# Kernel optimization log

Measured on AMD Instinct MI355X. Metric: run time of the kernel, lower is better.

## Reference

```python
import jax, jax.numpy as jnp
import numpy as np

A_DIM = 6
VBR = jnp.array([300.0, 750.0, 1200.0, 1850.0, 2850.0, 4300.0])
MAX_BR = 4300.0
BUF = 30000.0  # buffer_size fixed to 30000 each forward
N_STEPS = 6    # unrolled iterations in the source (cooked_bw[0]..cooked_bw[5])


def _conv_feat(x, w, b):
    # 1-channel valid Conv1d(kernel=4) + ReLU, flattened channel-major like torch .view
    L = x.shape[0]
    idx = jnp.arange(L - 3)[:, None] + jnp.arange(4)[None, :]
    win = x[idx]                                   # (L-3, 4)
    out = jax.nn.relu(win @ w[:, 0, :].T + b)      # (L-3, 128)
    return out.T.reshape(-1)                       # (128*(L-3),)


def setup_inputs() -> dict:
    key = jax.random.key(0)
    ks = jax.random.split(key, 12)
    s = 0.1
    return {
        "inp": jax.random.uniform(ks[0], (8, 8), jnp.float32) + 0.1,
        "conv_w": jax.random.normal(ks[1], (128, 1, 4), jnp.float32) * s,
        "conv_b": jax.random.normal(ks[2], (128,), jnp.float32) * s,
        "w0": jax.random.normal(ks[3], (128, 1), jnp.float32) * s,
        "b0": jax.random.normal(ks[4], (128,), jnp.float32) * s,
        "w1": jax.random.normal(ks[5], (128, 1), jnp.float32) * s,
        "b1": jax.random.normal(ks[6], (128,), jnp.float32) * s,
        "w2": jax.random.normal(ks[7], (128, 1), jnp.float32) * s,
        "b2": jax.random.normal(ks[8], (128,), jnp.float32) * s,
        "w3": jax.random.normal(ks[9], (128, 2048), jnp.float32) * 0.02,
        "b3": jax.random.normal(ks[10], (128,), jnp.float32) * s,
        "w4": jax.random.normal(ks[11], (6, 128), jnp.float32) * s,
        "b4": jnp.zeros((6,), jnp.float32),
    }


def reference(inp, conv_w, conv_b, w0, b0, w1, b1, w2, b2, w3, b3, w4, b4):
    state = inp[:6, :]          # (6, 8)
    bw = inp[6, :]              # cooked bandwidth trace
    vs = inp[7, 0]              # base video chunk size
    vcs = vs * jnp.array([1.0, 2.0, 4.0, 8.0, 16.0, 32.0])  # video_chunk_sizes

    def net(st):
        s0 = jax.nn.relu(st[0, -1] * w0[:, 0] + b0)
        s1 = jax.nn.relu(st[1, -1] * w1[:, 0] + b1)
        s2 = _conv_feat(st[2, :], conv_w, conv_b)          # 640
        s3 = _conv_feat(st[3, :], conv_w, conv_b)          # 640
        s4 = _conv_feat(st[4, :A_DIM], conv_w, conv_b)     # 384
        s5 = st[4, -1] * w2[:, 0] + b2                     # no relu (matches source)
        feat = jnp.concatenate([s0, s1, s2, s3, s4, s5])   # (2048,)
        h = jax.nn.relu(w3 @ feat + b3)
        return w4 @ h + b4                                 # (6,)

    for i in range(N_STEPS):
        logits = net(state)
        a = jnp.argmax(logits)
        state = jnp.roll(state, -1, axis=1)
        delay = vcs[a] / bw[i] - BUF
        state = state.at[0, -1].set(VBR[a] / MAX_BR)
        state = state.at[1, -1].set(BUF / 1000.0 / 10.0)
        state = state.at[2, -1].set(vcs[a] / delay / 1000.0)
        state = state.at[3, -1].set(delay / 1000.0 / 10.0)
        state = state.at[4, :A_DIM].set(vcs / 1e6)
        state = state.at[5, -1].set((7.0 - i) / 8.0)

    return net(state)
```

## Files before the change

kernel.cpp:

```cpp
#include <hip/hip_runtime.h>

#define NBLK 32
#define TPB  256
#define FSTRIDE 32
#define PSTRIDE 64

__device__ __forceinline__ float relu_(float x) { return fmaxf(x, 0.f); }


__launch_bounds__(TPB, 1)
__global__ void actor_kernel(
    const float* __restrict__ inp,
    const float* __restrict__ conv_w, const float* __restrict__ conv_b,
    const float* __restrict__ w0, const float* __restrict__ b0,
    const float* __restrict__ w1, const float* __restrict__ b1,
    const float* __restrict__ w2, const float* __restrict__ b2,
    const float* __restrict__ w3, const float* __restrict__ b3,
    const float* __restrict__ w4, const float* __restrict__ b4,
    float* __restrict__ out, int* __restrict__ flags,
    float* __restrict__ partials)
{
    const int tid = threadIdx.x;
    const int b   = blockIdx.x;

    __shared__ __align__(16) float lw3[4 * 2048];
    __shared__ __align__(16) float lfeat[2048];
    __shared__ __align__(16) float lc2[512], lc3[512];
    __shared__ float lbase2[128], lbase3[128], ls5[128];
    __shared__ float ls0[6 * 128];
    __shared__ float ltmp[512];
    __shared__ __align__(16) float lcw[512];
    __shared__ float lcb[128];
    __shared__ float lw0v[128], lb0v[128], lw1v[128], lb1v[128];
    __shared__ float lw2v[128], lb2v[128], lb3v[128];
    __shared__ float lw4[768], lb4v[8];
    __shared__ float st2[8], st3[8], st4[8];
    __shared__ float sx[8];
    __shared__ float lbw[8];
    __shared__ float h_lds[4], hv_lds[4 * 8];
    __shared__ float red[48];
    __shared__ float sval[32 * 48];
    __shared__ float s_red[192];
    __shared__ int   sact[2];

    {
        const float4* g4 = (const float4*)(w3 + b * 4 * 2048);
        float4* l4 = (float4*)lw3;
        for (int idx = tid; idx < 2048; idx += TPB) l4[idx] = g4[idx];
    }
    for (int idx = tid; idx < 512; idx += TPB) lcw[idx] = conv_w[idx];
    if (tid < 128) {
        lcb[tid]  = conv_b[tid];
        lw0v[tid] = w0[tid]; lb0v[tid] = b0[tid];
        lw1v[tid] = w1[tid]; lb1v[tid] = b1[tid];
        lw2v[tid] = w2[tid]; lb2v[tid] = b2[tid];
        lb3v[tid] = b3[tid];
    }
    for (int idx = tid; idx < 768; idx += TPB) lw4[idx] = w4[idx];
    if (tid < 6) lb4v[tid] = b4[tid];
    if (tid < 8) {
        st2[tid] = inp[16 + tid];
        st3[tid] = inp[24 + tid];
        st4[tid] = inp[32 + tid];
        lbw[tid] = inp[48 + tid];
    }
    if (tid == 0) {
        sx[0] = inp[7];   sx[1] = inp[15];
        sx[2] = inp[39];  sx[3] = inp[32];
        sx[4] = inp[56];
    }
    __syncthreads();

    if (tid < 128) {
        const float vb[6] = {300.f, 750.f, 1200.f, 1850.f, 2850.f, 4300.f};
        #pragma unroll
        for (int v = 0; v < 6; ++v)
            ls0[v * 128 + tid] = relu_(vb[v] * (1.f / 4300.f) * lw0v[tid] + lb0v[tid]);
        ltmp[tid] = relu_(3.0f * lw1v[tid] + lb1v[tid]);
    }
    for (int m = tid; m < 384; m += TPB) {
        int c = m / 3, w = m - c * 3;
        float a = lcb[c];
        #pragma unroll
        for (int k = 0; k < 4; ++k)
            a += sx[4] * (float)(1 << (w + k)) * 1e-6f * lcw[c * 4 + k];
        ltmp[128 + m] = relu_(a);
    }
    __syncthreads();

    const int wv = tid >> 6, lane = tid & 63;
    const float* wr = lw3 + wv * 2048;
    const float bias3 = lb3v[b * 4 + wv];

    float hs0p[6], hs14p;
    #pragma unroll
    for (int v = 0; v < 6; ++v)
        hs0p[v] = wr[lane] * ls0[v * 128 + lane] + wr[64 + lane] * ls0[v * 128 + 64 + lane];
    hs14p = wr[128 + lane] * ltmp[lane] + wr[192 + lane] * ltmp[64 + lane];
    #pragma unroll
    for (int k = 0; k < 6; ++k) {
        int m = lane + 64 * k;
        hs14p += wr[1536 + m] * ltmp[128 + m];
    }

    const float VBRc[6] = {300.f, 750.f, 1200.f, 1850.f, 2850.f, 4300.f};

    float fcom_f = 0.f;
    float lb2s[2], lb3s[2], b4f2[2], b4f3[2];
    float cw2s[2], cw3s[2], w32s[2], w33s[2], w42s[2], w43s[2];

    for (int g = 0; g < 3; ++g) {
        const int i = 2 * g;

        if (tid < 128) {
            lfeat[tid]        = relu_(sx[0] * lw0v[tid] + lb0v[tid]);
            lfeat[1920 + tid] =        sx[2] * lw2v[tid] + lb2v[tid];
            lbase2[tid] = st2[5] * lcw[tid*4] + st2[6] * lcw[tid*4+1]
                        + st2[7] * lcw[tid*4+2] + lcb[tid];
            lbase3[tid] = st3[5] * lcw[tid*4] + st3[6] * lcw[tid*4+1]
                        + st3[7] * lcw[tid*4+2] + lcb[tid];
            ls5[tid] = sx[3] * lw2v[tid] + lb2v[tid];
        } else {
            int j = tid - 128;
            lfeat[128 + j] = relu_(sx[1] * lw1v[j] + lb1v[j]);
        }
        for (int m = tid; m < 640; m += TPB) {
            int c = m / 5, w = m - c * 5;
            float a2 = lcb[c], a3 = lcb[c];
            #pragma unroll
            for (int k = 0; k < 4; ++k) {
                float cw = lcw[c * 4 + k];
                a2 += st2[w + k] * cw;
                a3 += st3[w + k] * cw;
            }
            lfeat[256 + m] = relu_(a2);
            lfeat[896 + m] = relu_(a3);
        }
        for (int m = tid; m < 384; m += TPB) {
            int c = m / 3, w = m - c * 3;
            float a4 = lcb[c];
            #pragma unroll
            for (int k = 0; k < 4; ++k) a4 += st4[w + k] * lcw[c * 4 + k];
            lfeat[1536 + m] = relu_(a4);
        }
        for (int m = tid; m < 512; m += TPB) {
            int c = m >> 2, w = m & 3;
            float a2 = lcb[c], a3 = lcb[c];
            #pragma unroll
            for (int k = 0; k < 4; ++k) {
                float cw = lcw[c * 4 + k];
                a2 += st2[w + 1 + k] * cw;
                a3 += st3[w + 1 + k] * cw;
            }
            lc2[m] = relu_(a2);
            lc3[m] = relu_(a3);
        }
        __syncthreads();

        float acc_i;
        {
            const float4* w4p = (const float4*)wr;
            const float4* f4p = (const float4*)lfeat;
            float4 acc = make_float4(0.f, 0.f, 0.f, 0.f);
            #pragma unroll
            for (int it = 0; it < 8; ++it) {
                float4 a = w4p[it * 64 + lane];
                float4 f = f4p[it * 64 + lane];
                acc.x += a.x * f.x; acc.y += a.y * f.y;
                acc.z += a.z * f.z; acc.w += a.w * f.w;
            }
            acc_i = (acc.x + acc.y) + (acc.z + acc.w);
        }

        float s5c = wr[1920 + lane] * ls5[lane] + wr[1984 + lane] * ls5[64 + lane];
        float acc_c = hs14p + s5c;
        #pragma unroll
        for (int k = 0; k < 8; ++k) {
            int m = lane + 64 * k;
            int col = 256 + (m >> 2) * 5 + (m & 3);
            acc_c += wr[col] * lc2[m] + wr[640 + col] * lc3[m];
        }

        float n2[6], n3[6];
        {
            float bwi = lbw[i], vs = sx[4];
            #pragma unroll
            for (int v = 0; v < 6; ++v) {
                float vca   = vs * (float)(1 << v);
                float delay = vca / bwi - 30000.f;
                n2[v] = vca / delay * 1e-3f;
                n3[v] = delay * 1e-4f;
            }
        }
        float accv[6];
        #pragma unroll
        for (int v = 0; v < 6; ++v) accv[v] = hs0p[v];
        #pragma unroll
        for (int t = 0; t < 2; ++t) {
            int c = lane + 64 * t;
            float cw3 = lcw[c * 4 + 3];
            float bb2 = lbase2[c], bb3 = lbase3[c];
            float wc2 = wr[256 + c * 5 + 4], wc3 = wr[896 + c * 5 + 4];
            #pragma unroll
            for (int v = 0; v < 6; ++v)
                accv[v] += relu_(bb2 + n2[v] * cw3) * wc2
                         + relu_(bb3 + n3[v] * cw3) * wc3;
        }

        if (g == 2) {
            fcom_f = hs14p + s5c;
            #pragma unroll
            for (int t = 0; t < 2; ++t) {
                int c = lane + 64 * t;
                float c0 = lcw[c*4], c1 = lcw[c*4+1], c2 = lcw[c*4+2], c3 = lcw[c*4+3];
                cw2s[t] = c2; cw3s[t] = c3;
                lb2s[t] = lbase2[c];  lb3s[t] = lbase3[c];
                b4f2[t] = st2[6]*c0 + st2[7]*c1 + lcb[c];
                b4f3[t] = st3[6]*c0 + st3[7]*c1 + lcb[c];
                w32s[t] = wr[256 + c*5 + 3]; w33s[t] = wr[896 + c*5 + 3];
                w42s[t] = wr[256 + c*5 + 4]; w43s[t] = wr[896 + c*5 + 4];
                #pragma unroll
                for (int w = 0; w < 3; ++w) {
                    float a2 = st2[2+w]*c0 + st2[3+w]*c1 + st2[4+w]*c2 + st2[5+w]*c3 + lcb[c];
                    float a3 = st3[2+w]*c0 + st3[3+w]*c1 + st3[4+w]*c2 + st3[5+w]*c3 + lcb[c];
                    fcom_f += relu_(a2) * wr[256 + c*5 + w] + relu_(a3) * wr[896 + c*5 + w];
                }
            }
        }

        #pragma unroll
        for (int off = 32; off > 0; off >>= 1) {
            acc_i += __shfl_xor(acc_i, off);
            acc_c += __shfl_xor(acc_c, off);
            #pragma unroll
            for (int v = 0; v < 6; ++v) accv[v] += __shfl_xor(accv[v], off);
        }
        if (lane == 0) {
            h_lds[wv] = relu_(acc_i + bias3);
            #pragma unroll
            for (int v = 0; v < 6; ++v)
                hv_lds[wv * 8 + v] = relu_(acc_c + accv[v] + bias3);
        }
        __syncthreads();

        if (tid < 42) {
            int q = tid / 6, t = tid - q * 6;
            float p = 0.f;
            if (q == 0) {
                #pragma unroll
                for (int w = 0; w < 4; ++w) p += lw4[t * 128 + b * 4 + w] * h_lds[w];
            } else {
                #pragma unroll
                for (int w = 0; w < 4; ++w) p += lw4[t * 128 + b * 4 + w] * hv_lds[w * 8 + (q - 1)];
            }
            __hip_atomic_store(&partials[(g * NBLK + b) * PSTRIDE + tid], p,
                               __ATOMIC_RELAXED, __HIP_MEMORY_SCOPE_AGENT);
        }
        __syncthreads();
        if (tid == 0)
            __hip_atomic_store(&flags[b * FSTRIDE], g + 1,
                               __ATOMIC_RELEASE, __HIP_MEMORY_SCOPE_AGENT);

        {
            const int bbs = tid >> 3;
            const int j   = tid & 7;
            while (__hip_atomic_load(&flags[bbs * FSTRIDE], __ATOMIC_ACQUIRE,
                                     __HIP_MEMORY_SCOPE_AGENT) < g + 1)
                __builtin_amdgcn_s_sleep(1);
            if (j < 7) {
                const float* src = &partials[(g * NBLK + bbs) * PSTRIDE + j * 6];
                #pragma unroll
                for (int k = 0; k < 6; ++k)
                    sval[bbs * 48 + j * 6 + k] =
                        __hip_atomic_load(&src[k], __ATOMIC_RELAXED,
                                          __HIP_MEMORY_SCOPE_AGENT);
            }
        }
        __syncthreads();
        if (tid < 42) {
            float p = lb4v[tid % 6];
            #pragma unroll
            for (int bb = 0; bb < NBLK; ++bb) p += sval[bb * 48 + tid];
            red[tid] = p;
        }
        __syncthreads();
        if (tid == 0) {
            float best = red[0]; int a0 = 0;
            #pragma unroll
            for (int r = 1; r < 6; ++r) if (red[r] > best) { best = red[r]; a0 = r; }
            best = red[6 + 6 * a0]; int a1 = 0;
            #pragma unroll
            for (int r = 1; r < 6; ++r)
                if (red[6 + 6 * a0 + r] > best) { best = red[6 + 6 * a0 + r]; a1 = r; }

            if (g == 2) {
                sact[0] = a0; sact[1] = a1;
            } else {
                {
                    float vca = sx[4] * (float)(1 << a0);
                    float delay = vca / lbw[i] - 30000.f;
                    sx[0] = VBRc[a0] * (1.f / 4300.f);
                    sx[1] = 3.0f;
                    #pragma unroll
                    for (int c = 0; c < 7; ++c) { st2[c] = st2[c + 1]; st3[c] = st3[c + 1]; }
                    st2[7] = vca / delay * 1e-3f;
                    st3[7] = delay * 1e-4f;
                    sx[2] = sx[3]; sx[3] = sx[4] * 1e-6f;
                    #pragma unroll
                    for (int j = 0; j < 6; ++j) st4[j] = sx[4] * (float)(1 << j) * 1e-6f;
                }
                {
                    float vca = sx[4] * (float)(1 << a1);
                    float delay = vca / lbw[i + 1] - 30000.f;
                    sx[0] = VBRc[a1] * (1.f / 4300.f);
                    sx[1] = 3.0f;
                    #pragma unroll
                    for (int c = 0; c < 7; ++c) { st2[c] = st2[c + 1]; st3[c] = st3[c + 1]; }
                    st2[7] = vca / delay * 1e-3f;
                    st3[7] = delay * 1e-4f;
                    sx[2] = sx[3]; sx[3] = sx[4] * 1e-6f;
                    #pragma unroll
                    for (int j = 0; j < 6; ++j) st4[j] = sx[4] * (float)(1 << j) * 1e-6f;
                }
            }
        }
        __syncthreads();
    }

    {
        const int a4 = sact[0], a5 = sact[1];
        float vs = sx[4];
        float vca4 = vs * (float)(1 << a4);
        float d4   = vca4 / lbw[4] - 30000.f;
        float ap24 = vca4 / d4 * 1e-3f, ap34 = d4 * 1e-4f;
        float vca5 = vs * (float)(1 << a5);
        float d5   = vca5 / lbw[5] - 30000.f;
        float ap25 = vca5 / d5 * 1e-3f, ap35 = d5 * 1e-4f;

        float h0 = hs0p[0];
        h0 = (a5 == 1) ? hs0p[1] : h0;
        h0 = (a5 == 2) ? hs0p[2] : h0;
        h0 = (a5 == 3) ? hs0p[3] : h0;
        h0 = (a5 == 4) ? hs0p[4] : h0;
        h0 = (a5 == 5) ? hs0p[5] : h0;

        float hl = fcom_f + h0;
        #pragma unroll
        for (int t = 0; t < 2; ++t) {
            float r32 = relu_(lb2s[t] + ap24 * cw3s[t]);
            float r33 = relu_(lb3s[t] + ap34 * cw3s[t]);
            float r42 = relu_(b4f2[t] + ap24 * cw2s[t] + ap25 * cw3s[t]);
            float r43 = relu_(b4f3[t] + ap34 * cw2s[t] + ap35 * cw3s[t]);
            hl += r32 * w32s[t] + r33 * w33s[t] + r42 * w42s[t] + r43 * w43s[t];
        }
        #pragma unroll
        for (int off = 32; off > 0; off >>= 1) hl += __shfl_xor(hl, off);
        if (lane == 0) h_lds[wv] = relu_(hl + bias3);
    }
    __syncthreads();
    if (tid < 6) {
        float p = 0.f;
        #pragma unroll
        for (int w = 0; w < 4; ++w) p += lw4[tid * 128 + b * 4 + w] * h_lds[w];
        __hip_atomic_store(&partials[(3 * NBLK + b) * PSTRIDE + tid], p,
                           __ATOMIC_RELAXED, __HIP_MEMORY_SCOPE_AGENT);
    }
    __syncthreads();
    if (tid == 0)
        __hip_atomic_store(&flags[b * FSTRIDE], 4,
                           __ATOMIC_RELEASE, __HIP_MEMORY_SCOPE_AGENT);
    if (b == 0) {
        if (tid < 192) {
            int j = tid >> 5, bb = tid & 31;
            while (__hip_atomic_load(&flags[bb * FSTRIDE], __ATOMIC_ACQUIRE,
                                     __HIP_MEMORY_SCOPE_AGENT) < 4)
                __builtin_amdgcn_s_sleep(1);
            s_red[j * 32 + bb] =
                __hip_atomic_load(&partials[(3 * NBLK + bb) * PSTRIDE + j],
                                  __ATOMIC_RELAXED, __HIP_MEMORY_SCOPE_AGENT);
        }
        __syncthreads();
        if (tid < 6) {
            float p = lb4v[tid];
            #pragma unroll
            for (int bb = 0; bb < NBLK; ++bb) p += s_red[tid * 32 + bb];
            out[tid] = p;
        }
    }
}

extern "C" void kernel_launch(void* const* d_in, const int* in_sizes, int n_in,
                              void* d_out, int out_size, void* d_ws, size_t ws_size,
                              hipStream_t stream) {
    const float* inp    = (const float*)d_in[0];
    const float* conv_w = (const float*)d_in[1];
    const float* conv_b = (const float*)d_in[2];
    const float* w0     = (const float*)d_in[3];
    const float* b0     = (const float*)d_in[4];
    const float* w1     = (const float*)d_in[5];
    const float* b1     = (const float*)d_in[6];
    const float* w2     = (const float*)d_in[7];
    const float* b2     = (const float*)d_in[8];
    const float* w3     = (const float*)d_in[9];
    const float* b3     = (const float*)d_in[10];
    const float* w4     = (const float*)d_in[11];
    const float* b4     = (const float*)d_in[12];

    int*   flags    = (int*)d_ws;
    float* partials = (float*)((char*)d_ws + 8192);

    actor_kernel<<<NBLK, TPB, 0, stream>>>(inp, conv_w, conv_b,
                                           w0, b0, w1, b1, w2, b2,
                                           w3, b3, w4, b4,
                                           (float*)d_out, flags, partials);
}
```

Baseline: 105.4 us.

## Replace flag-based inter-block sync with sequence-tagged 64-bit partial stores

Each block's partial logits are published as 64-bit words that pack the value with a step tag. Readers poll the tagged words directly instead of waiting on a per-block release flag and then reading the partials. This drops one __syncthreads, the flag store and a separate acquire round-trip per step, so each cross-block exchange takes fewer memory hops. The cost is that all 256 threads poll up to six scattered 64-bit words each, and correctness relies on the 64-bit relaxed atomic stores being observed whole and on stale workspace never holding a matching tag.

Result: faster. 98.95 us, median of 2 (-6.1%).

```diff
diff --git a/kernel.cpp b/kernel.cpp
--- a/kernel.cpp
+++ b/kernel.cpp
@@ -2,8 +2,7 @@
 
 #define NBLK 32
 #define TPB  256
-#define FSTRIDE 32
-#define PSTRIDE 64
+#define PSTRIDE64 64
 
 __device__ __forceinline__ float relu_(float x) { return fmaxf(x, 0.f); }
 
@@ -22,6 +21,8 @@
 {
     const int tid = threadIdx.x;
     const int b   = blockIdx.x;
+
+    unsigned long long* pub = (unsigned long long*)partials;
 
     __shared__ __align__(16) float lw3[4 * 2048];
     __shared__ __align__(16) float lfeat[2048];
@@ -40,7 +41,6 @@
     __shared__ float h_lds[4], hv_lds[4 * 8];
     __shared__ float red[48];
     __shared__ float sval[32 * 48];
-    __shared__ float s_red[192];
     __shared__ int   sact[2];
 
     {
@@ -104,6 +104,13 @@
     }
 
     const float VBRc[6] = {300.f, 750.f, 1200.f, 1850.f, 2850.f, 4300.f};
+
+    int tb[6], te[6], myN = 0;
+    #pragma unroll
+    for (int r = 0; r < 6; ++r) {
+        int idx = tid + 256 * r;
+        if (idx < 1344) { tb[myN] = idx / 42; te[myN] = idx - 42 * (idx / 42); ++myN; }
+    }
 
     float fcom_f = 0.f;
     float lb2s[2], lb3s[2], b4f2[2], b4f3[2];
@@ -253,30 +260,39 @@
                 #pragma unroll
                 for (int w = 0; w < 4; ++w) p += lw4[t * 128 + b * 4 + w] * hv_lds[w * 8 + (q - 1)];
             }
-            __hip_atomic_store(&partials[(g * NBLK + b) * PSTRIDE + tid], p,
+            union { float f[2]; unsigned long long u; } x;
+            x.f[0] = p; x.f[1] = (float)(g + 1);
+            __hip_atomic_store(&pub[(g * NBLK + b) * PSTRIDE64 + tid], x.u,
                                __ATOMIC_RELAXED, __HIP_MEMORY_SCOPE_AGENT);
         }
-        __syncthreads();
-        if (tid == 0)
-            __hip_atomic_store(&flags[b * FSTRIDE], g + 1,
-                               __ATOMIC_RELEASE, __HIP_MEMORY_SCOPE_AGENT);
 
         {
-            const int bbs = tid >> 3;
-            const int j   = tid & 7;
-            while (__hip_atomic_load(&flags[bbs * FSTRIDE], __ATOMIC_ACQUIRE,
-                                     __HIP_MEMORY_SCOPE_AGENT) < g + 1)
-                __builtin_amdgcn_s_sleep(1);
-            if (j < 7) {
-                const float* src = &partials[(g * NBLK + bbs) * PSTRIDE + j * 6];
+            const unsigned int seqbits = __float_as_uint((float)(g + 1));
+            unsigned int pend = (1u << myN) - 1u;
+            while (pend) {
+                unsigned long long v[6];
                 #pragma unroll
-                for (int k = 0; k < 6; ++k)
-                    sval[bbs * 48 + j * 6 + k] =
-                        __hip_atomic_load(&src[k], __ATOMIC_RELAXED,
-                                          __HIP_MEMORY_SCOPE_AGENT);
-            }
-        }
-        __syncthreads();
+                for (int k = 0; k < 6; ++k) {
+                    if (k < myN && (pend & (1u << k)))
+                        v[k] = __hip_atomic_load(
+                            &pub[(g * NBLK + tb[k]) * PSTRIDE64 + te[k]],
+                            __ATOMIC_RELAXED, __HIP_MEMORY_SCOPE_AGENT);
+                }
+                #pragma unroll
+                for (int k = 0; k < 6; ++k) {
+                    if (k < myN && (pend & (1u << k))) {
+                        if ((unsigned int)(v[k] >> 32) == seqbits) {
+                            sval[tb[k] * 48 + te[k]] =
+                                __uint_as_float((unsigned int)(v[k] & 0xFFFFFFFFu));
+                            pend &= ~(1u << k);
+                        }
+                    }
+                }
+                if (pend) __builtin_amdgcn_s_sleep(1);
+            }
+        }
+        __syncthreads();
+
         if (tid < 42) {
             float p = lb4v[tid % 6];
             #pragma unroll
@@ -358,32 +374,37 @@
         if (lane == 0) h_lds[wv] = relu_(hl + bias3);
     }
     __syncthreads();
+
     if (tid < 6) {
         float p = 0.f;
         #pragma unroll
         for (int w = 0; w < 4; ++w) p += lw4[tid * 128 + b * 4 + w] * h_lds[w];
-        __hip_atomic_store(&partials[(3 * NBLK + b) * PSTRIDE + tid], p,
+        union { float f[2]; unsigned long long u; } x;
+        x.f[0] = p; x.f[1] = 4.0f;
+        __hip_atomic_store(&pub[(3 * NBLK + b) * PSTRIDE64 + tid], x.u,
                            __ATOMIC_RELAXED, __HIP_MEMORY_SCOPE_AGENT);
     }
-    __syncthreads();
-    if (tid == 0)
-        __hip_atomic_store(&flags[b * FSTRIDE], 4,
-                           __ATOMIC_RELEASE, __HIP_MEMORY_SCOPE_AGENT);
     if (b == 0) {
         if (tid < 192) {
-            int j = tid >> 5, bb = tid & 31;
-            while (__hip_atomic_load(&flags[bb * FSTRIDE], __ATOMIC_ACQUIRE,
-                                     __HIP_MEMORY_SCOPE_AGENT) < 4)
+            int bb = tid / 6, e = tid - 6 * bb;
+            const unsigned int seqbits = __float_as_uint(4.0f);
+            for (;;) {
+                unsigned long long u = __hip_atomic_load(
+                    &pub[(3 * NBLK + bb) * PSTRIDE64 + e],
+                    __ATOMIC_RELAXED, __HIP_MEMORY_SCOPE_AGENT);
+                if ((unsigned int)(u >> 32) == seqbits) {
+                    sval[bb * 48 + e] =
+                        __uint_as_float((unsigned int)(u & 0xFFFFFFFFu));
+                    break;
+                }
                 __builtin_amdgcn_s_sleep(1);
-            s_red[j * 32 + bb] =
-                __hip_atomic_load(&partials[(3 * NBLK + bb) * PSTRIDE + j],
-                                  __ATOMIC_RELAXED, __HIP_MEMORY_SCOPE_AGENT);
+            }
         }
         __syncthreads();
         if (tid < 6) {
             float p = lb4v[tid];
             #pragma unroll
-            for (int bb = 0; bb < NBLK; ++bb) p += s_red[tid * 32 + bb];
+            for (int bb = 0; bb < NBLK; ++bb) p += sval[bb * 48 + tid];
             out[tid] = p;
         }
     }
```
